# Kernel tuning notes

Measured on AMD Instinct MI355X. Metric: run time of the kernel, lower is better.

## Reference

```python
import jax, jax.numpy as jnp
import numpy as np

N, IN_DIM, HID, OUT, NH = 512, 256, 256, 256, 4
HD = OUT // NH  # head_dim = 64
EPS = 1e-5


def _mlp(x, w1, b1, w2, b2):
    return jax.nn.relu(x @ w1 + b1) @ w2 + b2


def setup_inputs() -> dict:
    key = jax.random.key(0)
    ks = jax.random.split(key, 32)

    def rn(k, shape, fan_in):
        return (jax.random.normal(k, shape, jnp.float32) / np.float32(np.sqrt(fan_in)))

    V = jax.random.normal(ks[0], (N, IN_DIM), jnp.float32)
    adj = jax.random.randint(ks[1], (N, N), 0, 2, jnp.int32)
    adj = adj.at[jnp.arange(N), jnp.arange(N)].set(1)  # self-edges: avoid all -inf rows
    prev_hidden = jax.random.normal(ks[2], (N, HID), jnp.float32)
    z = jnp.zeros
    return dict(
        V=V, adj=adj, prev_hidden=prev_hidden,
        W1=rn(ks[3], (IN_DIM, HID), IN_DIM),
        a_std0=rn(ks[4], (HID, 1), HID), a_std1=rn(ks[5], (HID, 1), HID),
        ce_w1=rn(ks[6], (2 * IN_DIM, HID), 2 * IN_DIM), ce_b1=z((HID,), jnp.float32),
        ce_w2=rn(ks[7], (HID, HD), HID), ce_b2=z((HD,), jnp.float32),
        a_c0=rn(ks[8], (HD, 1), HD), a_c1=rn(ks[9], (HD, 1), HD),
        te_w1=rn(ks[10], (IN_DIM + HID, HID), IN_DIM + HID), te_b1=z((HID,), jnp.float32),
        te_w2=rn(ks[11], (HID, HD), HID), te_b2=z((HD,), jnp.float32),
        a_t0=rn(ks[12], (HD, 1), HD), a_t1=rn(ks[13], (HD, 1), HD),
        co_w1=rn(ks[14], (3 * IN_DIM, HID), 3 * IN_DIM), co_b1=z((HID,), jnp.float32),
        co_w2=rn(ks[15], (HID, HD), HID), co_b2=z((HD,), jnp.float32),
        a_co0=rn(ks[16], (HD, 1), HD), a_co1=rn(ks[17], (HD, 1), HD),
        W2=rn(ks[18], (HID + 2 * HD + 1, OUT), HID + 2 * HD + 1),
        Wo=rn(ks[19], (OUT, OUT), OUT), bo=z((OUT,), jnp.float32),
        ln_g=jnp.ones((OUT,), jnp.float32), ln_b=z((OUT,), jnp.float32),
    )


def reference(V, adj, prev_hidden, W1, a_std0, a_std1,
              ce_w1, ce_b1, ce_w2, ce_b2, a_c0, a_c1,
              te_w1, te_b1, te_w2, te_b2, a_t0, a_t1,
              co_w1, co_b1, co_w2, co_b2, a_co0, a_co1,
              W2, Wo, bo, ln_g, ln_b):
    ninf = -jnp.inf

    # ---- standard GAT branch -> H1: (N, HID) ----
    Wh1 = V @ W1
    s1 = Wh1 @ a_std0 + (Wh1 @ a_std1).T                      # (N, N)
    s1 = jnp.where(adj == 0, ninf, s1)
    H1 = jax.nn.softmax(s1, axis=1) @ Wh1

    # ---- causal branch: all ordered pairs i!=j, global softmax -> H2: (N, HD) ----
    pair = jnp.concatenate([jnp.broadcast_to(V[:, None, :], (N, N, IN_DIM)),
                            jnp.broadcast_to(V[None, :, :], (N, N, IN_DIM))], axis=-1)
    cf = _mlp(pair, ce_w1, ce_b1, ce_w2, ce_b2)               # (N, N, HD)
    cs = (cf @ (a_c0 + a_c1))[..., 0]                         # (N, N)
    cs = jnp.where(jnp.eye(N, dtype=bool), ninf, cs)          # exclude i==j pairs
    ca = jax.nn.softmax(cs.reshape(-1)).reshape(N, N, 1)
    H2 = jnp.broadcast_to((ca * cf).sum((0, 1)), (N, HD))

    # ---- temporal branch: (N,1) scores broadcast against causal mask -> running mean ----
    tf = _mlp(jnp.concatenate([V, prev_hidden], axis=-1), te_w1, te_b1, te_w2, te_b2)  # (N, HD)
    ts = tf @ (a_t0 + a_t1)                                   # (N, 1)
    cmask = jnp.triu(jnp.ones((N, N), bool), 1)
    tsb = jnp.where(cmask, ninf, jnp.broadcast_to(ts, (N, N)))
    H3 = jax.nn.softmax(tsb, axis=1) @ tf                     # (N, HD)

    # ---- coop branch: first two neighbors by index; size-1 softmax; buggy pad -> (N,1) ----
    order = jnp.argsort((1 - adj).astype(jnp.int32), axis=1, stable=True)  # adj==1 first, index order
    nb = V[order[:, :2]]                                      # (N, 2, IN_DIM)
    valid = ((adj == 1).sum(axis=1) >= 2)
    nb = jnp.where(valid[:, None, None], nb, jnp.zeros_like(nb))
    ci = jnp.concatenate([V, nb[:, 0], nb[:, 1]], axis=-1)    # (N, 3*IN_DIM)
    cf4 = _mlp(ci, co_w1, co_b1, co_w2, co_b2)                # (N, HD)
    ca4 = jax.nn.softmax(cf4 @ (a_co0 + a_co1), axis=1)       # (N,1): softmax over size-1 -> ones
    h4vec = (ca4.T @ cf4)[0]                                  # (HD,)
    # original: squeeze(-2)->(HD,), dim==1 -> unsqueeze(-1)->(HD,1), zero-pad rows to N
    H4 = jnp.zeros((N, 1), V.dtype).at[:HD, 0].set(h4vec)

    # ---- combine, lazy W2, proj, LN, ELU (dropout identity in eval) ----
    Hc = jnp.concatenate([H1, H2, H3, H4], axis=-1) @ W2      # (N, OUT)
    out = Hc @ Wo + bo
    mu = out.mean(-1, keepdims=True)
    var = ((out - mu) ** 2).mean(-1, keepdims=True)
    out = (out - mu) / jnp.sqrt(var + EPS) * ln_g + ln_b
    return jax.nn.elu(out)
```

## Files before the change

### kernel.cpp

```cpp
#include <hip/hip_runtime.h>
#include <math.h>

#define NN 512
#define HD 64
#define EPSV 1e-5f

typedef unsigned short u16;
typedef short s4v __attribute__((ext_vector_type(4)));
typedef short s8v __attribute__((ext_vector_type(8)));
typedef float f4v __attribute__((ext_vector_type(4)));

struct GD {
  const float *A, *A2, *A3, *A4;
  const int* I;
  const float *B, *bias;
  float* C;
  int M, K, Nn, mode, act;
};

#define GEMM_SMEM 28800
#define MEGA_SMEM 38656

__device__ __forceinline__ void split_bf16(float x, u16& h, u16& l) {
  unsigned xb = __float_as_uint(x);
  float hf = __uint_as_float(xb & 0xffff0000u);
  h = (u16)(xb >> 16);
  l = (u16)(__float_as_uint(x - hf) >> 16);
}

__device__ __forceinline__ void gemm_body(char* smem, const GD& d, int bx, int by) {
  u16 (*Ah)[72] = (u16(*)[72])smem;
  u16 (*Al)[72] = (u16(*)[72])(smem + 4608);
  u16 (*Bh)[68] = (u16(*)[68])(smem + 9216);
  u16 (*Bl)[68] = (u16(*)[68])(smem + 9216 + 8704);
  char* extra = smem + 26624;
  int* nbl = (int*)extra;
  float* wscl = (float*)extra;
  float* rowsuml = wscl + 512;

  const int t = threadIdx.x;
  const int rowbase = by * 32, colbase = bx * 64;
  const int K = d.K, Nn = d.Nn, mode = d.mode, M = d.M;
  if (rowbase >= M) return;

  if (mode == 2) {
    int wave = t >> 6, lane = t & 63;
    for (int rr = wave; rr < 32; rr += 4) {
      int row = rowbase + rr;
      int n0 = -1, n1 = -1, cnt = 0;
      for (int c = 0; c < 8; ++c) {
        unsigned long long mm = __ballot(d.I[row * NN + c * 64 + lane] != 0);
        cnt += (int)__popcll(mm);
        if (n0 < 0 && mm) { n0 = c * 64 + (int)__builtin_ctzll(mm); mm &= mm - 1; }
        if (n1 < 0 && mm) { n1 = c * 64 + (int)__builtin_ctzll(mm); }
      }
      if (lane == 0) { nbl[rr * 3] = n0; nbl[rr * 3 + 1] = n1; nbl[rr * 3 + 2] = (cnt >= 2); }
    }
    __syncthreads();
  } else if (mode == 4) {
    wscl[t] = d.A2[t];
    wscl[256 + t] = d.A2[256 + t];
    __syncthreads();
  }

  float4 aR[2], bR[4];
  float rs0 = 0.f, rs1 = 0.f;

  auto loadA = [&](int k0) {
#pragma unroll
    for (int j = 0; j < 2; ++j) {
      int idx = t + j * 256;
      int r = idx >> 4, c0 = (idx & 15) * 4;
      int row = rowbase + r, gk = k0 + c0;
      float4 v4 = make_float4(0.f, 0.f, 0.f, 0.f);
      if (mode == 0) {
        if (row < M && gk < K) v4 = *(const float4*)&d.A[(size_t)row * K + gk];
      } else if (mode == 1) {
        if (gk < 256) v4 = *(const float4*)&d.A[row * 256 + gk];
        else v4 = *(const float4*)&d.A2[row * 256 + gk - 256];
      } else if (mode == 2) {
        int seg = gk >> 8;
        int src = (seg == 0) ? row : (nbl[r * 3 + 2] ? nbl[r * 3 + seg - 1] : -1);
        if (src >= 0) v4 = *(const float4*)&d.A[src * 256 + (gk & 255)];
      } else if (mode == 3) {
        if (gk + 3 < 256) v4 = *(const float4*)&d.A[row * 256 + gk];
        else if (gk >= 256 && gk + 3 < 320) v4 = *(const float4*)&d.A2[gk - 256];
        else if (gk >= 320 && gk + 3 < 384) v4 = *(const float4*)&d.A3[row * 64 + gk - 320];
        else if (gk == 384) v4.x = (row < 64) ? d.A4[row] : 0.f;
      } else {
        int4 a4 = *(const int4*)&d.I[row * NN + gk];
        v4.x = a4.x ? wscl[gk + 0] : 0.f;
        v4.y = a4.y ? wscl[gk + 1] : 0.f;
        v4.z = a4.z ? wscl[gk + 2] : 0.f;
        v4.w = a4.w ? wscl[gk + 3] : 0.f;
        float ss = v4.x + v4.y + v4.z + v4.w;
        if (j == 0) rs0 += ss; else rs1 += ss;
      }
      aR[j] = v4;
    }
  };
  auto loadB = [&](int k0) {
#pragma unroll
    for (int j = 0; j < 4; ++j) {
      int idx = t + j * 256;
      int r = idx >> 4, c0 = (idx & 15) * 4;
      int gk = k0 + r;
      float4 v4 = make_float4(0.f, 0.f, 0.f, 0.f);
      if (gk < K) v4 = *(const float4*)&d.B[(size_t)gk * Nn + colbase + c0];
      bR[j] = v4;
    }
  };
  auto stos = [&]() {
#pragma unroll
    for (int j = 0; j < 2; ++j) {
      int idx = t + j * 256;
      int r = idx >> 4, c0 = (idx & 15) * 4;
      float v[4] = {aR[j].x, aR[j].y, aR[j].z, aR[j].w};
      u16 h[4], l[4];
#pragma unroll
      for (int e = 0; e < 4; ++e) split_bf16(v[e], h[e], l[e]);
      *(short4*)&Ah[r][c0] = make_short4(h[0], h[1], h[2], h[3]);
      *(short4*)&Al[r][c0] = make_short4(l[0], l[1], l[2], l[3]);
    }
#pragma unroll
    for (int j = 0; j < 4; ++j) {
      int idx = t + j * 256;
      int r = idx >> 4, c0 = (idx & 15) * 4;
      float v[4] = {bR[j].x, bR[j].y, bR[j].z, bR[j].w};
#pragma unroll
      for (int e = 0; e < 4; ++e) {
        u16 h, l;
        split_bf16(v[e], h, l);
        Bh[c0 + e][r] = h;
        Bl[c0 + e][r] = l;
      }
    }
  };

  f4v acc0 = {0.f, 0.f, 0.f, 0.f};
  f4v acc1 = {0.f, 0.f, 0.f, 0.f};

  const int w4 = t >> 6;
  const int lrow = t & 15;
  const int lk = ((t & 63) >> 4) * 8;

  int iters = (K + 63) >> 6;
  loadA(0); loadB(0);
  for (int it = 0; it < iters; ++it) {
    stos();
    __syncthreads();
    if (it + 1 < iters) { loadA((it + 1) << 6); loadB((it + 1) << 6); }
    const u16* bhrow = Bh[w4 * 16 + lrow];
    const u16* blrow = Bl[w4 * 16 + lrow];
#pragma unroll
    for (int ks = 0; ks < 2; ++ks) {
      int ko = ks * 32 + lk;
      s4v bh_0 = *(const s4v*)&bhrow[ko];
      s4v bh_1 = *(const s4v*)&bhrow[ko + 4];
      s4v bl_0 = *(const s4v*)&blrow[ko];
      s4v bl_1 = *(const s4v*)&blrow[ko + 4];
      s8v bh = __builtin_shufflevector(bh_0, bh_1, 0, 1, 2, 3, 4, 5, 6, 7);
      s8v bl = __builtin_shufflevector(bl_0, bl_1, 0, 1, 2, 3, 4, 5, 6, 7);
      {
        s8v ah = *(const s8v*)&Ah[lrow][ko];
        s8v al = *(const s8v*)&Al[lrow][ko];
        acc0 = __builtin_amdgcn_mfma_f32_16x16x32_bf16(ah, bh, acc0, 0, 0, 0);
        acc0 = __builtin_amdgcn_mfma_f32_16x16x32_bf16(ah, bl, acc0, 0, 0, 0);
        acc0 = __builtin_amdgcn_mfma_f32_16x16x32_bf16(al, bh, acc0, 0, 0, 0);
      }
      {
        s8v ah = *(const s8v*)&Ah[16 + lrow][ko];
        s8v al = *(const s8v*)&Al[16 + lrow][ko];
        acc1 = __builtin_amdgcn_mfma_f32_16x16x32_bf16(ah, bh, acc1, 0, 0, 0);
        acc1 = __builtin_amdgcn_mfma_f32_16x16x32_bf16(ah, bl, acc1, 0, 0, 0);
        acc1 = __builtin_amdgcn_mfma_f32_16x16x32_bf16(al, bh, acc1, 0, 0, 0);
      }
    }
    __syncthreads();
  }

  if (mode == 4) {
    float a0 = rs0, a1 = rs1;
#pragma unroll
    for (int off = 8; off; off >>= 1) {
      a0 += __shfl_xor(a0, off, 16);
      a1 += __shfl_xor(a1, off, 16);
    }
    if ((t & 15) == 0) { rowsuml[t >> 4] = a0; rowsuml[16 + (t >> 4)] = a1; }
    __syncthreads();
  }

  int col = colbase + w4 * 16 + lrow;
  float bvs = d.bias ? d.bias[col] : 0.f;
  int qrow = ((t & 63) >> 4) * 4;
#pragma unroll
  for (int m = 0; m < 2; ++m) {
#pragma unroll
    for (int q = 0; q < 4; ++q) {
      int lr = m * 16 + qrow + q;
      int row = rowbase + lr;
      if (row >= M) continue;
      float o = (m ? acc1[q] : acc0[q]) + bvs;
      if (d.act) o = fmaxf(o, 0.f);
      if (mode == 4) o *= (1.f / rowsuml[lr]);
      d.C[(size_t)row * Nn + col] = o;
    }
  }
}

__device__ void wsc_body(char* smem, const float* W1, const float* a_std1,
                         const float* V, float* expwsc, int grp) {
  float* asl = (float*)smem;
  float* ul  = asl + 256;
  int t = threadIdx.x;
  asl[t] = a_std1[t];
  __syncthreads();
  {
    float s = 0.f;
    const float* wr = W1 + t * 256;
    for (int h = 0; h < 256; h += 4) {
      float4 w4 = *(const float4*)&wr[h];
      float4 a4 = *(const float4*)&asl[h];
      s += w4.x * a4.x + w4.y * a4.y + w4.z * a4.z + w4.w * a4.w;
    }
    ul[t] = s;
  }
  __syncthreads();
  int wave = t >> 6, lane = t & 63;
  float4 u4 = *(const float4*)&ul[lane * 4];
  int j0 = grp * 128;
  for (int j = j0 + wave; j < j0 + 128; j += 4) {
    float4 v4 = *(const float4*)&V[j * 256 + lane * 4];
    float s = v4.x * u4.x + v4.y * u4.y + v4.z * u4.z + v4.w * u4.w;
#pragma unroll
    for (int off = 32; off; off >>= 1) s += __shfl_xor(s, off, 64);
    if (lane == 0) expwsc[j] = __expf(s);
  }
}

struct GD7 { GD d[7]; };
__global__ __launch_bounds__(256) void gemm7_k(GD7 ds) {
  __shared__ __align__(16) char smem[GEMM_SMEM];
  int z = blockIdx.z;
  if (z == 6) {
    if (blockIdx.y != 0) return;
    wsc_body(smem, ds.d[6].A, ds.d[6].A2, ds.d[6].A3, ds.d[6].C, blockIdx.x);
    return;
  }
  gemm_body(smem, ds.d[z], blockIdx.x, blockIdx.y);
}
__global__ __launch_bounds__(256) void gemm1_k(GD d) {
  __shared__ __align__(16) char smem[GEMM_SMEM];
  gemm_body(smem, d, blockIdx.x, blockIdx.y);
}

__device__ void pair_body(char* smem,
    const float* __restrict__ P, const float* __restrict__ Q,
    const float* __restrict__ b1, const float* __restrict__ ce_w2,
    const float* __restrict__ a_c0, const float* __restrict__ a_c1,
    float* __restrict__ mpart, float* __restrict__ dpart,
    float* __restrict__ spart, int byy, int bxx) {
  float* Pl  = (float*)smem;
  float* Ql  = Pl + 16 * 260;
  float* el  = Ql + 16 * 260;
  float* wcl = el + 16 * 20;
  float* red = wcl + 256;
  float* sk  = red + 256;
  float* sbl = sk + 256;
  int t = threadIdx.x;

  if (t < 64) red[t] = a_c0[t] + a_c1[t];
  __syncthreads();
  {
    float s = 0.f;
    const float* w2r = ce_w2 + t * 64;
#pragma unroll 8
    for (int h = 0; h < 64; ++h) s += w2r[h] * red[h];
    wcl[t] = s;
  }
  int i0 = byy * 16, j0 = bxx * 16;
  for (int e = t; e < 1024; e += 256) {
    int r = e >> 6, c4 = (e & 63) * 4;
    float4 bb = *(const float4*)&b1[c4];
    float4 pv = *(const float4*)&P[(i0 + r) * 256 + c4];
    pv.x += bb.x; pv.y += bb.y; pv.z += bb.z; pv.w += bb.w;
    *(float4*)&Pl[r * 260 + c4] = pv;
    *(float4*)&Ql[r * 260 + c4] = *(const float4*)&Q[(j0 + r) * 256 + c4];
  }
  __syncthreads();

  int a = t >> 4, b = t & 15;
  const float* pr = &Pl[a * 260];
  const float* qr = &Ql[b * 260];
  float4 c4a = make_float4(0.f, 0.f, 0.f, 0.f);
#pragma unroll 8
  for (int k4 = 0; k4 < 64; ++k4) {
    float4 w = *(const float4*)&wcl[k4 * 4];
    float4 p = *(const float4*)&pr[k4 * 4];
    float4 q = *(const float4*)&qr[k4 * 4];
    c4a.x += fmaxf(p.x + q.x, 0.f) * w.x;
    c4a.y += fmaxf(p.y + q.y, 0.f) * w.y;
    c4a.z += fmaxf(p.z + q.z, 0.f) * w.z;
    c4a.w += fmaxf(p.w + q.w, 0.f) * w.w;
  }
  float s = c4a.x + c4a.y + c4a.z + c4a.w;
  if (i0 + a == j0 + b) s = -INFINITY;
  red[t] = s; __syncthreads();
  for (int ss = 128; ss; ss >>= 1) { if (t < ss) red[t] = fmaxf(red[t], red[t + ss]); __syncthreads(); }
  float mb = red[0];
  __syncthreads();
  float e = __expf(s - mb);
  el[a * 20 + b] = e;
  red[t] = e; __syncthreads();
  for (int ss = 128; ss; ss >>= 1) { if (t < ss) red[t] += red[t + ss]; __syncthreads(); }
  float db = red[0];
  __syncthreads();

  float qv[16];
#pragma unroll
  for (int j = 0; j < 16; ++j) qv[j] = Ql[j * 260 + t];
  float rk = 0.f;
#pragma unroll 4
  for (int i = 0; i < 16; ++i) {
    float pv = Pl[i * 260 + t];
    const float* erow = &el[i * 20];
#pragma unroll
    for (int j4 = 0; j4 < 4; ++j4) {
      float4 e4 = *(const float4*)&erow[j4 * 4];
      rk += e4.x * fmaxf(pv + qv[j4 * 4 + 0], 0.f);
      rk += e4.y * fmaxf(pv + qv[j4 * 4 + 1], 0.f);
      rk += e4.z * fmaxf(pv + qv[j4 * 4 + 2], 0.f);
      rk += e4.w * fmaxf(pv + qv[j4 * 4 + 3], 0.f);
    }
  }
  sk[t] = rk;
  __syncthreads();
  {
    int h = t & 63, q = t >> 6;
    float s2 = 0.f;
    for (int k = q * 64; k < q * 64 + 64; ++k) s2 += sk[k] * ce_w2[k * 64 + h];
    sbl[q * 64 + h] = s2;
  }
  __syncthreads();
  int blk = byy * 32 + bxx;
  if (t < 64) spart[blk * 64 + t] = sbl[t] + sbl[64 + t] + sbl[128 + t] + sbl[192 + t];
  if (t == 0) { mpart[blk] = mb; dpart[blk] = db; }
}

struct MegaArgs {
  const float *P, *Q, *b1, *ce_w2, *a_c0, *a_c1;
  float *mpart, *dpart, *spart;
  GD gH1, gTf, gCf;
};

__global__ __launch_bounds__(256) void mega_k(MegaArgs a) {
  __shared__ __align__(16) char smem[MEGA_SMEM];
  int b = blockIdx.x;
  if (b < 64) {
    gemm_body(smem, a.gH1, b & 3, b >> 2);
  } else if (b < 80) {
    gemm_body(smem, a.gTf, 0, b - 64);
  } else if (b < 96) {
    gemm_body(smem, a.gCf, 0, b - 80);
  } else {
    int p = b - 96;
    pair_body(smem, a.P, a.Q, a.b1, a.ce_w2, a.a_c0, a.a_c1,
              a.mpart, a.dpart, a.spart, p >> 5, p & 31);
  }
}

__global__ __launch_bounds__(1024) void mini_k(
    const float* __restrict__ mpart, const float* __restrict__ dpart,
    const float* __restrict__ spart, const float* __restrict__ ce_b2,
    float* __restrict__ H2row,
    const float* __restrict__ tf, float* __restrict__ H3,
    const float* __restrict__ cf4, float* __restrict__ h4vec) {
  __shared__ float A[1024];
  __shared__ float Bsh[1024];
  __shared__ float segsum[16][65];
  int b = blockIdx.x, t = threadIdx.x;
  if (b == 0) {
    float mv = mpart[t];
    A[t] = mv; __syncthreads();
    for (int s = 512; s; s >>= 1) { if (t < s) A[t] = fmaxf(A[t], A[t + s]); __syncthreads(); }
    float M = A[0];
    __syncthreads();
    float e = __expf(mv - M);
    Bsh[t] = e;
    A[t] = e * dpart[t];
    __syncthreads();
    for (int s = 512; s; s >>= 1) { if (t < s) A[t] += A[t + s]; __syncthreads(); }
    float D = A[0];
    __syncthreads();
    int h = t & 63, g = t >> 6;
    float s2 = 0.f;
    for (int b2 = g * 64; b2 < g * 64 + 64; ++b2) s2 += Bsh[b2] * spart[b2 * 64 + h];
    A[t] = s2;
    __syncthreads();
    for (int p = 8; p; p >>= 1) { if (g < p) A[g * 64 + h] += A[(g + p) * 64 + h]; __syncthreads(); }
    if (t < 64) H2row[t] = A[t] / D + ce_b2[t];
  } else if (b == 1) {
    int h = t & 63, g = t >> 6;
    float vals[32];
    float run = 0.f;
#pragma unroll
    for (int r = 0; r < 32; ++r) { run += tf[(g * 32 + r) * 64 + h]; vals[r] = run; }
    segsum[g][h] = run;
    __syncthreads();
    float off = 0.f;
    for (int gg = 0; gg < g; ++gg) off += segsum[gg][h];
#pragma unroll
    for (int r = 0; r < 32; ++r) {
      int i = g * 32 + r;
      H3[i * 64 + h] = (vals[r] + off) / (float)(i + 1);
    }
  } else {
    int h = t & 63, g = t >> 6;
    float s = 0.f;
    for (int r = 0; r < 32; ++r) s += cf4[(g * 32 + r) * 64 + h];
    A[g * 64 + h] = s;
    __syncthreads();
    for (int p = 8; p; p >>= 1) { if (g < p) A[g * 64 + h] += A[(g + p) * 64 + h]; __syncthreads(); }
    if (t < 64) h4vec[t] = A[t];
  }
}

__global__ void ln_elu_kernel(const float* __restrict__ X, const float* __restrict__ g,
                              const float* __restrict__ b, float* __restrict__ out) {
  __shared__ float red[256];
  int i = blockIdx.x, tid = threadIdx.x;
  float x = X[i * 256 + tid];
  red[tid] = x; __syncthreads();
  for (int s = 128; s; s >>= 1) { if (tid < s) red[tid] += red[tid + s]; __syncthreads(); }
  float mu = red[0] * (1.f / 256.f);
  __syncthreads();
  float d = x - mu;
  red[tid] = d * d; __syncthreads();
  for (int s = 128; s; s >>= 1) { if (tid < s) red[tid] += red[tid + s]; __syncthreads(); }
  float var = red[0] * (1.f / 256.f);
  float y = d / sqrtf(var + EPSV) * g[tid] + b[tid];
  out[i * 256 + tid] = (y > 0.f) ? y : (expf(y) - 1.f);
}

static GD mkgd(const float* A, const float* A2, const float* A3, const float* A4,
               const int* I, const float* B, const float* bias, float* C,
               int M, int K, int Nn, int mode, int act) {
  GD g{A, A2, A3, A4, I, B, bias, C, M, K, Nn, mode, act};
  return g;
}

extern "C" void kernel_launch(void* const* d_in, const int* in_sizes, int n_in,
                              void* d_out, int out_size, void* d_ws, size_t ws_size,
                              hipStream_t stream) {
  const float* V      = (const float*)d_in[0];
  const int*   adj    = (const int*)  d_in[1];
  const float* ph     = (const float*)d_in[2];
  const float* W1     = (const float*)d_in[3];
  const float* a_std1 = (const float*)d_in[5];
  const float* ce_w1  = (const float*)d_in[6];
  const float* ce_b1  = (const float*)d_in[7];
  const float* ce_w2  = (const float*)d_in[8];
  const float* ce_b2  = (const float*)d_in[9];
  const float* a_c0   = (const float*)d_in[10];
  const float* a_c1   = (const float*)d_in[11];
  const float* te_w1  = (const float*)d_in[12];
  const float* te_b1  = (const float*)d_in[13];
  const float* te_w2  = (const float*)d_in[14];
  const float* te_b2  = (const float*)d_in[15];
  const float* co_w1  = (const float*)d_in[18];
  const float* co_b1  = (const float*)d_in[19];
  const float* co_w2  = (const float*)d_in[20];
  const float* co_b2  = (const float*)d_in[21];
  const float* W2     = (const float*)d_in[24];
  const float* Wo     = (const float*)d_in[25];
  const float* bo     = (const float*)d_in[26];
  const float* ln_g   = (const float*)d_in[27];
  const float* ln_b   = (const float*)d_in[28];
  float* out = (float*)d_out;

  float* ws = (float*)d_ws;
  size_t off = 0;
  auto alloc = [&](size_t n) { float* p = ws + off; off += (n + 15) & ~(size_t)15; return p; };

  float* Wh1    = alloc(512 * 256);
  float* Pb     = alloc(512 * 256);
  float* Qb     = alloc(512 * 256);
  float* tfh    = alloc(512 * 256);
  float* cf4h   = alloc(512 * 256);
  float* H1     = alloc(512 * 256);
  float* Wfused = alloc(385 * 256);
  float* T2     = alloc(512 * 256);
  float* tf     = alloc(512 * 64);
  float* cf4    = alloc(512 * 64);
  float* H3     = alloc(512 * 64);
  float* spart  = alloc(1024 * 64);
  float* mpart  = alloc(1024);
  float* dpart  = alloc(1024);
  float* expwsc = alloc(512);
  float* H2row  = alloc(64);
  float* h4vec  = alloc(64);
  (void)ws_size; (void)in_sizes; (void)n_in; (void)out_size;

  GD7 sA;
  sA.d[0] = mkgd(V, 0, 0, 0, 0, W1, 0, Wh1, 512, 256, 256, 0, 0);
  sA.d[1] = mkgd(V, 0, 0, 0, 0, ce_w1, 0, Pb, 512, 256, 256, 0, 0);
  sA.d[2] = mkgd(V, 0, 0, 0, 0, ce_w1 + 256 * 256, 0, Qb, 512, 256, 256, 0, 0);
  sA.d[3] = mkgd(V, ph, 0, 0, 0, te_w1, te_b1, tfh, 512, 512, 256, 1, 1);
  sA.d[4] = mkgd(V, 0, 0, 0, adj, co_w1, co_b1, cf4h, 512, 768, 256, 2, 1);
  sA.d[5] = mkgd(W2, 0, 0, 0, 0, Wo, 0, Wfused, 385, 256, 256, 0, 0);
  sA.d[6] = mkgd(W1, a_std1, V, 0, 0, 0, 0, expwsc, 512, 256, 1, 6, 0);
  gemm7_k<<<dim3(4, 16, 7), 256, 0, stream>>>(sA);

  MegaArgs ma;
  ma.P = Pb; ma.Q = Qb; ma.b1 = ce_b1; ma.ce_w2 = ce_w2;
  ma.a_c0 = a_c0; ma.a_c1 = a_c1;
  ma.mpart = mpart; ma.dpart = dpart; ma.spart = spart;
  ma.gH1 = mkgd(0, expwsc, 0, 0, adj, Wh1, 0, H1, 512, 512, 256, 4, 0);
  ma.gTf = mkgd(tfh, 0, 0, 0, 0, te_w2, te_b2, tf, 512, 256, 64, 0, 0);
  ma.gCf = mkgd(cf4h, 0, 0, 0, 0, co_w2, co_b2, cf4, 512, 256, 64, 0, 0);
  mega_k<<<1120, 256, 0, stream>>>(ma);

  mini_k<<<3, 1024, 0, stream>>>(mpart, dpart, spart, ce_b2, H2row, tf, H3, cf4, h4vec);

  GD gF = mkgd(H1, H2row, H3, h4vec, 0, Wfused, bo, T2, 512, 385, 256, 3, 0);
  gemm1_k<<<dim3(4, 16), 256, 0, stream>>>(gF);

  ln_elu_kernel<<<512, 256, 0, stream>>>(T2, ln_g, ln_b, out);
}
```

Baseline: 193.7 us.

## Fuse mini and LN kernels via atomic last-block, pre-split transposed bf16 weights

```diff
diff --git a/kernel.cpp b/kernel.cpp
--- a/kernel.cpp
+++ b/kernel.cpp
@@ -15,6 +15,9 @@
   const int* I;
   const float *B, *bias;
   float* C;
+  const u16 *Bth, *Btl;
+  u16 *Cth, *Ctl;
+  int Bkp, Ckp;
   int M, K, Nn, mode, act;
 };
 
@@ -64,6 +67,7 @@
   }
 
   float4 aR[2], bR[4];
+  s8v bp[4];
   float rs0 = 0.f, rs1 = 0.f;
 
   auto loadA = [&](int k0) {
@@ -100,14 +104,25 @@
     }
   };
   auto loadB = [&](int k0) {
-#pragma unroll
-    for (int j = 0; j < 4; ++j) {
-      int idx = t + j * 256;
-      int r = idx >> 4, c0 = (idx & 15) * 4;
-      int gk = k0 + r;
-      float4 v4 = make_float4(0.f, 0.f, 0.f, 0.f);
-      if (gk < K) v4 = *(const float4*)&d.B[(size_t)gk * Nn + colbase + c0];
-      bR[j] = v4;
+    if (d.Bth) {
+#pragma unroll
+      for (int j = 0; j < 2; ++j) {
+        int idx = t + j * 256;
+        int n = idx >> 3, kb = (idx & 7) * 8;
+        size_t base = (size_t)(colbase + n) * d.Bkp + k0 + kb;
+        bp[j] = *(const s8v*)&d.Bth[base];
+        bp[2 + j] = *(const s8v*)&d.Btl[base];
+      }
+    } else {
+#pragma unroll
+      for (int j = 0; j < 4; ++j) {
+        int idx = t + j * 256;
+        int r = idx >> 4, c0 = (idx & 15) * 4;
+        int gk = k0 + r;
+        float4 v4 = make_float4(0.f, 0.f, 0.f, 0.f);
+        if (gk < K) v4 = *(const float4*)&d.B[(size_t)gk * Nn + colbase + c0];
+        bR[j] = v4;
+      }
     }
   };
   auto stos = [&]() {
@@ -119,20 +134,30 @@
       u16 h[4], l[4];
 #pragma unroll
       for (int e = 0; e < 4; ++e) split_bf16(v[e], h[e], l[e]);
-      *(short4*)&Ah[r][c0] = make_short4(h[0], h[1], h[2], h[3]);
-      *(short4*)&Al[r][c0] = make_short4(l[0], l[1], l[2], l[3]);
-    }
-#pragma unroll
-    for (int j = 0; j < 4; ++j) {
-      int idx = t + j * 256;
-      int r = idx >> 4, c0 = (idx & 15) * 4;
-      float v[4] = {bR[j].x, bR[j].y, bR[j].z, bR[j].w};
-#pragma unroll
-      for (int e = 0; e < 4; ++e) {
-        u16 h, l;
-        split_bf16(v[e], h, l);
-        Bh[c0 + e][r] = h;
-        Bl[c0 + e][r] = l;
+      *(short4*)&Ah[r][c0] = make_short4((short)h[0], (short)h[1], (short)h[2], (short)h[3]);
+      *(short4*)&Al[r][c0] = make_short4((short)l[0], (short)l[1], (short)l[2], (short)l[3]);
+    }
+    if (d.Bth) {
+#pragma unroll
+      for (int j = 0; j < 2; ++j) {
+        int idx = t + j * 256;
+        int n = idx >> 3, kb = (idx & 7) * 8;
+        *(s8v*)&Bh[n][kb] = bp[j];
+        *(s8v*)&Bl[n][kb] = bp[2 + j];
+      }
+    } else {
+#pragma unroll
+      for (int j = 0; j < 4; ++j) {
+        int idx = t + j * 256;
+        int r = idx >> 4, c0 = (idx & 15) * 4;
+        float v[4] = {bR[j].x, bR[j].y, bR[j].z, bR[j].w};
+#pragma unroll
+        for (int e = 0; e < 4; ++e) {
+          u16 h, l;
+          split_bf16(v[e], h, l);
+          Bh[c0 + e][r] = h;
+          Bl[c0 + e][r] = l;
+        }
       }
     }
   };
@@ -191,19 +216,32 @@
   }
 
   int col = colbase + w4 * 16 + lrow;
-  float bvs = d.bias ? d.bias[col] : 0.f;
   int qrow = ((t & 63) >> 4) * 4;
-#pragma unroll
-  for (int m = 0; m < 2; ++m) {
-#pragma unroll
-    for (int q = 0; q < 4; ++q) {
-      int lr = m * 16 + qrow + q;
-      int row = rowbase + lr;
-      if (row >= M) continue;
-      float o = (m ? acc1[q] : acc0[q]) + bvs;
-      if (d.act) o = fmaxf(o, 0.f);
-      if (mode == 4) o *= (1.f / rowsuml[lr]);
-      d.C[(size_t)row * Nn + col] = o;
+  if (d.Cth) {
+    size_t cb = (size_t)col * d.Ckp + rowbase + qrow;
+#pragma unroll
+    for (int m = 0; m < 2; ++m) {
+      u16 hh[4], ll[4];
+#pragma unroll
+      for (int q = 0; q < 4; ++q) split_bf16(m ? acc1[q] : acc0[q], hh[q], ll[q]);
+      *(short4*)&d.Cth[cb + m * 16] = make_short4((short)hh[0], (short)hh[1], (short)hh[2], (short)hh[3]);
+      *(short4*)&d.Ctl[cb + m * 16] = make_short4((short)ll[0], (short)ll[1], (short)ll[2], (short)ll[3]);
+    }
+  }
+  if (d.C) {
+    float bvs = d.bias ? d.bias[col] : 0.f;
+#pragma unroll
+    for (int m = 0; m < 2; ++m) {
+#pragma unroll
+      for (int q = 0; q < 4; ++q) {
+        int lr = m * 16 + qrow + q;
+        int row = rowbase + lr;
+        if (row >= M) continue;
+        float o = (m ? acc1[q] : acc0[q]) + bvs;
+        if (d.act) o = fmaxf(o, 0.f);
+        if (mode == 4) o *= (1.f / rowsuml[lr]);
+        d.C[(size_t)row * Nn + col] = o;
+      }
     }
   }
 }
@@ -238,26 +276,71 @@
   }
 }
 
-struct GD7 { GD d[7]; };
+struct GD7 {
+  GD d[7];
+  const float *tw2, *cw2, *ce_w2, *a_c0, *a_c1;
+  u16 *tw2h, *tw2l, *cw2h, *cw2l, *wfh, *wfl;
+  float* wclg;
+  unsigned* cnts;
+};
+
+__device__ void conv_body(char* smem, int bx, const GD7& a) {
+  float (*Ls)[66] = (float(*)[66])smem;
+  int t = threadIdx.x;
+  const float* src = (bx < 2) ? a.tw2 : a.cw2;
+  u16* dh = (bx < 2) ? a.tw2h : a.cw2h;
+  u16* dl = (bx < 2) ? a.tw2l : a.cw2l;
+  int k0 = (bx & 1) * 128;
+  for (int kt = 0; kt < 2; ++kt) {
+    int k00 = k0 + kt * 64;
+#pragma unroll
+    for (int j = 0; j < 4; ++j) {
+      int idx = t + j * 256;
+      int r = idx >> 4, c = (idx & 15) * 4;
+      *(float4*)&Ls[r][c] = *(const float4*)&src[(k00 + r) * 64 + c];
+    }
+    __syncthreads();
+#pragma unroll
+    for (int j = 0; j < 4; ++j) {
+      int idx = t + j * 256;
+      int n = idx >> 4, kk = (idx & 15) * 4;
+      u16 hh[4], ll[4];
+#pragma unroll
+      for (int e = 0; e < 4; ++e) split_bf16(Ls[kk + e][n], hh[e], ll[e]);
+      *(short4*)&dh[n * 256 + k00 + kk] = make_short4((short)hh[0], (short)hh[1], (short)hh[2], (short)hh[3]);
+      *(short4*)&dl[n * 256 + k00 + kk] = make_short4((short)ll[0], (short)ll[1], (short)ll[2], (short)ll[3]);
+    }
+    __syncthreads();
+  }
+  if (bx == 3) {
+    if (t < 36) a.cnts[t] = 0u;
+    float s = 0.f;
+    const float* w2r = a.ce_w2 + t * 64;
+    for (int h = 0; h < 64; ++h) s += w2r[h] * (a.a_c0[h] + a.a_c1[h]);
+    a.wclg[t] = s;
+    int n = t;
+    for (int kk = 416; kk < 448; kk += 4) {
+      *(short4*)&a.wfh[n * 448 + kk] = make_short4(0, 0, 0, 0);
+      *(short4*)&a.wfl[n * 448 + kk] = make_short4(0, 0, 0, 0);
+    }
+  }
+}
+
 __global__ __launch_bounds__(256) void gemm7_k(GD7 ds) {
   __shared__ __align__(16) char smem[GEMM_SMEM];
   int z = blockIdx.z;
   if (z == 6) {
-    if (blockIdx.y != 0) return;
-    wsc_body(smem, ds.d[6].A, ds.d[6].A2, ds.d[6].A3, ds.d[6].C, blockIdx.x);
+    if (blockIdx.y == 0) { wsc_body(smem, ds.d[6].A, ds.d[6].A2, ds.d[6].A3, ds.d[6].C, blockIdx.x); return; }
+    if (blockIdx.y == 1) { conv_body(smem, blockIdx.x, ds); return; }
     return;
   }
   gemm_body(smem, ds.d[z], blockIdx.x, blockIdx.y);
-}
-__global__ __launch_bounds__(256) void gemm1_k(GD d) {
-  __shared__ __align__(16) char smem[GEMM_SMEM];
-  gemm_body(smem, d, blockIdx.x, blockIdx.y);
 }
 
 __device__ void pair_body(char* smem,
     const float* __restrict__ P, const float* __restrict__ Q,
     const float* __restrict__ b1, const float* __restrict__ ce_w2,
-    const float* __restrict__ a_c0, const float* __restrict__ a_c1,
+    const float* __restrict__ wclg,
     float* __restrict__ mpart, float* __restrict__ dpart,
     float* __restrict__ spart, int byy, int bxx) {
   float* Pl  = (float*)smem;
@@ -269,15 +352,7 @@
   float* sbl = sk + 256;
   int t = threadIdx.x;
 
-  if (t < 64) red[t] = a_c0[t] + a_c1[t];
-  __syncthreads();
-  {
-    float s = 0.f;
-    const float* w2r = ce_w2 + t * 64;
-#pragma unroll 8
-    for (int h = 0; h < 64; ++h) s += w2r[h] * red[h];
-    wcl[t] = s;
-  }
+  wcl[t] = wclg[t];
   int i0 = byy * 16, j0 = bxx * 16;
   for (int e = t; e < 1024; e += 256) {
     int r = e >> 6, c4 = (e & 63) * 4;
@@ -305,16 +380,20 @@
   }
   float s = c4a.x + c4a.y + c4a.z + c4a.w;
   if (i0 + a == j0 + b) s = -INFINITY;
-  red[t] = s; __syncthreads();
-  for (int ss = 128; ss; ss >>= 1) { if (t < ss) red[t] = fmaxf(red[t], red[t + ss]); __syncthreads(); }
-  float mb = red[0];
-  __syncthreads();
+  float wm = s;
+#pragma unroll
+  for (int off = 32; off; off >>= 1) wm = fmaxf(wm, __shfl_xor(wm, off, 64));
+  if ((t & 63) == 0) red[t >> 6] = wm;
+  __syncthreads();
+  float mb = fmaxf(fmaxf(red[0], red[1]), fmaxf(red[2], red[3]));
   float e = __expf(s - mb);
   el[a * 20 + b] = e;
-  red[t] = e; __syncthreads();
-  for (int ss = 128; ss; ss >>= 1) { if (t < ss) red[t] += red[t + ss]; __syncthreads(); }
-  float db = red[0];
-  __syncthreads();
+  float ws2 = e;
+#pragma unroll
+  for (int off = 32; off; off >>= 1) ws2 += __shfl_xor(ws2, off, 64);
+  if ((t & 63) == 0) red[8 + (t >> 6)] = ws2;
+  __syncthreads();
+  float db = red[8] + red[9] + red[10] + red[11];
 
   float qv[16];
 #pragma unroll
@@ -348,104 +427,143 @@
 }
 
 struct MegaArgs {
-  const float *P, *Q, *b1, *ce_w2, *a_c0, *a_c1;
+  const float *P, *Q, *b1, *ce_w2, *wclg;
   float *mpart, *dpart, *spart;
+  const float *ce_b2; float *H2row;
+  const float *tf; float *H3;
+  const float *cf4; float *h4vec;
+  unsigned* cnts;
   GD gH1, gTf, gCf;
 };
+
+__device__ void mini_job(char* smem, int job, const MegaArgs& a) {
+  float* Ash = (float*)smem;
+  float* Bsh = Ash + 256;
+  int t = threadIdx.x;
+  int h = t & 63, g = t >> 6;
+  if (job == 0) {
+    float mv[4];
+    float m0 = -INFINITY;
+#pragma unroll
+    for (int i = 0; i < 4; ++i) { mv[i] = a.mpart[t + i * 256]; m0 = fmaxf(m0, mv[i]); }
+    Ash[t] = m0; __syncthreads();
+    for (int s = 128; s; s >>= 1) { if (t < s) Ash[t] = fmaxf(Ash[t], Ash[t + s]); __syncthreads(); }
+    float M = Ash[0]; __syncthreads();
+    float d0 = 0.f;
+#pragma unroll
+    for (int i = 0; i < 4; ++i) {
+      float e = __expf(mv[i] - M);
+      Bsh[t + i * 256] = e;
+      d0 += e * a.dpart[t + i * 256];
+    }
+    Ash[t] = d0; __syncthreads();
+    for (int s = 128; s; s >>= 1) { if (t < s) Ash[t] += Ash[t + s]; __syncthreads(); }
+    float D = Ash[0]; __syncthreads();
+    float s2 = 0.f;
+    for (int b2 = g * 256; b2 < g * 256 + 256; ++b2) s2 += Bsh[b2] * a.spart[b2 * 64 + h];
+    Ash[t] = s2; __syncthreads();
+    if (g == 0) {
+      float r = Ash[h] + Ash[64 + h] + Ash[128 + h] + Ash[192 + h];
+      a.H2row[h] = r / D + a.ce_b2[h];
+    }
+  } else if (job == 1) {
+    float run = 0.f;
+    for (int r = 0; r < 128; ++r) run += a.tf[(g * 128 + r) * 64 + h];
+    Ash[g * 64 + h] = run; __syncthreads();
+    float off = 0.f;
+    for (int gg = 0; gg < g; ++gg) off += Ash[gg * 64 + h];
+    float run2 = off;
+    for (int r = 0; r < 128; ++r) {
+      int i = g * 128 + r;
+      run2 += a.tf[i * 64 + h];
+      a.H3[i * 64 + h] = run2 / (float)(i + 1);
+    }
+  } else {
+    float s = 0.f;
+    for (int r = 0; r < 128; ++r) s += a.cf4[(g * 128 + r) * 64 + h];
+    Ash[g * 64 + h] = s; __syncthreads();
+    if (g == 0) a.h4vec[h] = Ash[h] + Ash[64 + h] + Ash[128 + h] + Ash[192 + h];
+  }
+}
 
 __global__ __launch_bounds__(256) void mega_k(MegaArgs a) {
   __shared__ __align__(16) char smem[MEGA_SMEM];
   int b = blockIdx.x;
   if (b < 64) {
     gemm_body(smem, a.gH1, b & 3, b >> 2);
-  } else if (b < 80) {
-    gemm_body(smem, a.gTf, 0, b - 64);
   } else if (b < 96) {
-    gemm_body(smem, a.gCf, 0, b - 80);
+    int isTf = (b < 80);
+    gemm_body(smem, isTf ? a.gTf : a.gCf, 0, isTf ? (b - 64) : (b - 80));
+    __syncthreads();
+    __threadfence();
+    __shared__ unsigned po;
+    if (threadIdx.x == 0) po = atomicAdd(&a.cnts[isTf ? 17 : 18], 1u);
+    __syncthreads();
+    if (po == 15u) { __threadfence(); mini_job(smem, isTf ? 1 : 2, a); }
   } else {
     int p = b - 96;
-    pair_body(smem, a.P, a.Q, a.b1, a.ce_w2, a.a_c0, a.a_c1,
+    pair_body(smem, a.P, a.Q, a.b1, a.ce_w2, a.wclg,
               a.mpart, a.dpart, a.spart, p >> 5, p & 31);
-  }
-}
-
-__global__ __launch_bounds__(1024) void mini_k(
-    const float* __restrict__ mpart, const float* __restrict__ dpart,
-    const float* __restrict__ spart, const float* __restrict__ ce_b2,
-    float* __restrict__ H2row,
-    const float* __restrict__ tf, float* __restrict__ H3,
-    const float* __restrict__ cf4, float* __restrict__ h4vec) {
-  __shared__ float A[1024];
-  __shared__ float Bsh[1024];
-  __shared__ float segsum[16][65];
-  int b = blockIdx.x, t = threadIdx.x;
-  if (b == 0) {
-    float mv = mpart[t];
-    A[t] = mv; __syncthreads();
-    for (int s = 512; s; s >>= 1) { if (t < s) A[t] = fmaxf(A[t], A[t + s]); __syncthreads(); }
-    float M = A[0];
-    __syncthreads();
-    float e = __expf(mv - M);
-    Bsh[t] = e;
-    A[t] = e * dpart[t];
-    __syncthreads();
-    for (int s = 512; s; s >>= 1) { if (t < s) A[t] += A[t + s]; __syncthreads(); }
-    float D = A[0];
-    __syncthreads();
-    int h = t & 63, g = t >> 6;
-    float s2 = 0.f;
-    for (int b2 = g * 64; b2 < g * 64 + 64; ++b2) s2 += Bsh[b2] * spart[b2 * 64 + h];
-    A[t] = s2;
-    __syncthreads();
-    for (int p = 8; p; p >>= 1) { if (g < p) A[g * 64 + h] += A[(g + p) * 64 + h]; __syncthreads(); }
-    if (t < 64) H2row[t] = A[t] / D + ce_b2[t];
-  } else if (b == 1) {
-    int h = t & 63, g = t >> 6;
-    float vals[32];
-    float run = 0.f;
-#pragma unroll
-    for (int r = 0; r < 32; ++r) { run += tf[(g * 32 + r) * 64 + h]; vals[r] = run; }
-    segsum[g][h] = run;
-    __syncthreads();
-    float off = 0.f;
-    for (int gg = 0; gg < g; ++gg) off += segsum[gg][h];
-#pragma unroll
-    for (int r = 0; r < 32; ++r) {
-      int i = g * 32 + r;
-      H3[i * 64 + h] = (vals[r] + off) / (float)(i + 1);
-    }
-  } else {
-    int h = t & 63, g = t >> 6;
-    float s = 0.f;
-    for (int r = 0; r < 32; ++r) s += cf4[(g * 32 + r) * 64 + h];
-    A[g * 64 + h] = s;
-    __syncthreads();
-    for (int p = 8; p; p >>= 1) { if (g < p) A[g * 64 + h] += A[(g + p) * 64 + h]; __syncthreads(); }
-    if (t < 64) h4vec[t] = A[t];
-  }
-}
-
-__global__ void ln_elu_kernel(const float* __restrict__ X, const float* __restrict__ g,
-                              const float* __restrict__ b, float* __restrict__ out) {
-  __shared__ float red[256];
-  int i = blockIdx.x, tid = threadIdx.x;
-  float x = X[i * 256 + tid];
-  red[tid] = x; __syncthreads();
-  for (int s = 128; s; s >>= 1) { if (tid < s) red[tid] += red[tid + s]; __syncthreads(); }
-  float mu = red[0] * (1.f / 256.f);
-  __syncthreads();
-  float d = x - mu;
-  red[tid] = d * d; __syncthreads();
-  for (int s = 128; s; s >>= 1) { if (tid < s) red[tid] += red[tid + s]; __syncthreads(); }
-  float var = red[0] * (1.f / 256.f);
-  float y = d / sqrtf(var + EPSV) * g[tid] + b[tid];
-  out[i * 256 + tid] = (y > 0.f) ? y : (expf(y) - 1.f);
+    __syncthreads();
+    __threadfence();
+    __shared__ unsigned po;
+    if (threadIdx.x == 0) {
+      unsigned fin = 0xffffffffu;
+      unsigned g1 = atomicAdd(&a.cnts[20 + (p >> 6)], 1u);
+      if (g1 == 63u) fin = atomicAdd(&a.cnts[16], 1u);
+      po = fin;
+    }
+    __syncthreads();
+    if (po == 15u) { __threadfence(); mini_job(smem, 0, a); }
+  }
+}
+
+__global__ __launch_bounds__(256) void gemm_ln_k(GD d, const float* __restrict__ lng,
+                                                 const float* __restrict__ lnb,
+                                                 float* __restrict__ out, unsigned* cnts) {
+  __shared__ __align__(16) char smem[GEMM_SMEM];
+  gemm_body(smem, d, blockIdx.x, blockIdx.y);
+  __syncthreads();
+  __threadfence();
+  __shared__ unsigned po;
+  if (threadIdx.x == 0) po = atomicAdd(&cnts[blockIdx.y], 1u);
+  __syncthreads();
+  if (po == 3u) {
+    __threadfence();
+    int t = threadIdx.x, lane = t & 63, w = t >> 6;
+    const float* T2 = d.C;
+    for (int r8 = 0; r8 < 8; ++r8) {
+      int row = blockIdx.y * 32 + w * 8 + r8;
+      float4 x = *(const float4*)&T2[row * 256 + lane * 4];
+      float s = x.x + x.y + x.z + x.w;
+#pragma unroll
+      for (int off = 32; off; off >>= 1) s += __shfl_xor(s, off, 64);
+      float mu = s * (1.f / 256.f);
+      float4 dv = make_float4(x.x - mu, x.y - mu, x.z - mu, x.w - mu);
+      float s2 = dv.x * dv.x + dv.y * dv.y + dv.z * dv.z + dv.w * dv.w;
+#pragma unroll
+      for (int off = 32; off; off >>= 1) s2 += __shfl_xor(s2, off, 64);
+      float rstd = 1.f / sqrtf(s2 * (1.f / 256.f) + EPSV);
+      float4 gg = *(const float4*)&lng[lane * 4];
+      float4 bb = *(const float4*)&lnb[lane * 4];
+      float4 y;
+      y.x = dv.x * rstd * gg.x + bb.x;
+      y.y = dv.y * rstd * gg.y + bb.y;
+      y.z = dv.z * rstd * gg.z + bb.z;
+      y.w = dv.w * rstd * gg.w + bb.w;
+      y.x = (y.x > 0.f) ? y.x : (expf(y.x) - 1.f);
+      y.y = (y.y > 0.f) ? y.y : (expf(y.y) - 1.f);
+      y.z = (y.z > 0.f) ? y.z : (expf(y.z) - 1.f);
+      y.w = (y.w > 0.f) ? y.w : (expf(y.w) - 1.f);
+      *(float4*)&out[row * 256 + lane * 4] = y;
+    }
+  }
 }
 
 static GD mkgd(const float* A, const float* A2, const float* A3, const float* A4,
                const int* I, const float* B, const float* bias, float* C,
                int M, int K, int Nn, int mode, int act) {
-  GD g{A, A2, A3, A4, I, B, bias, C, M, K, Nn, mode, act};
+  GD g{A, A2, A3, A4, I, B, bias, C, 0, 0, 0, 0, 0, 0, M, K, Nn, mode, act};
   return g;
 }
 
@@ -482,13 +600,11 @@
   size_t off = 0;
   auto alloc = [&](size_t n) { float* p = ws + off; off += (n + 15) & ~(size_t)15; return p; };
 
-  float* Wh1    = alloc(512 * 256);
   float* Pb     = alloc(512 * 256);
   float* Qb     = alloc(512 * 256);
   float* tfh    = alloc(512 * 256);
   float* cf4h   = alloc(512 * 256);
   float* H1     = alloc(512 * 256);
-  float* Wfused = alloc(385 * 256);
   float* T2     = alloc(512 * 256);
   float* tf     = alloc(512 * 64);
   float* cf4    = alloc(512 * 64);
@@ -499,31 +615,48 @@
   float* expwsc = alloc(512);
   float* H2row  = alloc(64);
   float* h4vec  = alloc(64);
+  u16* Wh1t_h = (u16*)alloc(65536);
+  u16* Wh1t_l = (u16*)alloc(65536);
+  u16* Wf_h   = (u16*)alloc(57344);
+  u16* Wf_l   = (u16*)alloc(57344);
+  u16* tw2h   = (u16*)alloc(8192);
+  u16* tw2l   = (u16*)alloc(8192);
+  u16* cw2h   = (u16*)alloc(8192);
+  u16* cw2l   = (u16*)alloc(8192);
+  float* wclg = alloc(256);
+  unsigned* cnts = (unsigned*)alloc(64);
   (void)ws_size; (void)in_sizes; (void)n_in; (void)out_size;
 
   GD7 sA;
-  sA.d[0] = mkgd(V, 0, 0, 0, 0, W1, 0, Wh1, 512, 256, 256, 0, 0);
+  sA.d[0] = mkgd(V, 0, 0, 0, 0, W1, 0, 0, 512, 256, 256, 0, 0);
+  sA.d[0].Cth = Wh1t_h; sA.d[0].Ctl = Wh1t_l; sA.d[0].Ckp = 512;
   sA.d[1] = mkgd(V, 0, 0, 0, 0, ce_w1, 0, Pb, 512, 256, 256, 0, 0);
   sA.d[2] = mkgd(V, 0, 0, 0, 0, ce_w1 + 256 * 256, 0, Qb, 512, 256, 256, 0, 0);
   sA.d[3] = mkgd(V, ph, 0, 0, 0, te_w1, te_b1, tfh, 512, 512, 256, 1, 1);
   sA.d[4] = mkgd(V, 0, 0, 0, adj, co_w1, co_b1, cf4h, 512, 768, 256, 2, 1);
-  sA.d[5] = mkgd(W2, 0, 0, 0, 0, Wo, 0, Wfused, 385, 256, 256, 0, 0);
+  sA.d[5] = mkgd(W2, 0, 0, 0, 0, Wo, 0, 0, 385, 256, 256, 0, 0);
+  sA.d[5].Cth = Wf_h; sA.d[5].Ctl = Wf_l; sA.d[5].Ckp = 448;
   sA.d[6] = mkgd(W1, a_std1, V, 0, 0, 0, 0, expwsc, 512, 256, 1, 6, 0);
+  sA.tw2 = te_w2; sA.cw2 = co_w2; sA.ce_w2 = ce_w2; sA.a_c0 = a_c0; sA.a_c1 = a_c1;
+  sA.tw2h = tw2h; sA.tw2l = tw2l; sA.cw2h = cw2h; sA.cw2l = cw2l;
+  sA.wfh = Wf_h; sA.wfl = Wf_l; sA.wclg = wclg; sA.cnts = cnts;
   gemm7_k<<<dim3(4, 16, 7), 256, 0, stream>>>(sA);
 
   MegaArgs ma;
-  ma.P = Pb; ma.Q = Qb; ma.b1 = ce_b1; ma.ce_w2 = ce_w2;
-  ma.a_c0 = a_c0; ma.a_c1 = a_c1;
+  ma.P = Pb; ma.Q = Qb; ma.b1 = ce_b1; ma.ce_w2 = ce_w2; ma.wclg = wclg;
   ma.mpart = mpart; ma.dpart = dpart; ma.spart = spart;
-  ma.gH1 = mkgd(0, expwsc, 0, 0, adj, Wh1, 0, H1, 512, 512, 256, 4, 0);
-  ma.gTf = mkgd(tfh, 0, 0, 0, 0, te_w2, te_b2, tf, 512, 256, 64, 0, 0);
-  ma.gCf = mkgd(cf4h, 0, 0, 0, 0, co_w2, co_b2, cf4, 512, 256, 64, 0, 0);
+  ma.ce_b2 = ce_b2; ma.H2row = H2row;
+  ma.tf = tf; ma.H3 = H3; ma.cf4 = cf4; ma.h4vec = h4vec;
+  ma.cnts = cnts;
+  ma.gH1 = mkgd(0, expwsc, 0, 0, adj, 0, 0, H1, 512, 512, 256, 4, 0);
+  ma.gH1.Bth = Wh1t_h; ma.gH1.Btl = Wh1t_l; ma.gH1.Bkp = 512;
+  ma.gTf = mkgd(tfh, 0, 0, 0, 0, 0, te_b2, tf, 512, 256, 64, 0, 0);
+  ma.gTf.Bth = tw2h; ma.gTf.Btl = tw2l; ma.gTf.Bkp = 256;
+  ma.gCf = mkgd(cf4h, 0, 0, 0, 0, 0, co_b2, cf4, 512, 256, 64, 0, 0);
+  ma.gCf.Bth = cw2h; ma.gCf.Btl = cw2l; ma.gCf.Bkp = 256;
   mega_k<<<1120, 256, 0, stream>>>(ma);
 
-  mini_k<<<3, 1024, 0, stream>>>(mpart, dpart, spart, ce_b2, H2row, tf, H3, cf4, h4vec);
-
-  GD gF = mkgd(H1, H2row, H3, h4vec, 0, Wfused, bo, T2, 512, 385, 256, 3, 0);
-  gemm1_k<<<dim3(4, 16), 256, 0, stream>>>(gF);
-
-  ln_elu_kernel<<<512, 256, 0, stream>>>(T2, ln_g, ln_b, out);
-}
+  GD gF = mkgd(H1, H2row, H3, h4vec, 0, 0, bo, T2, 512, 385, 256, 3, 0);
+  gF.Bth = Wf_h; gF.Btl = Wf_l; gF.Bkp = 448;
+  gemm_ln_k<<<dim3(4, 16), 256, 0, stream>>>(gF, ln_g, ln_b, out, cnts);
+}
```

Measured after the change: 325.5 us. +68.1%, slower.
